# Performance work log

Measured on AMD Instinct MI355X. Metric: run time of the kernel, lower is better.

## Reference

```python
import jax, jax.numpy as jnp
import numpy as np

B, N, D = 32, 512, 256   # sets, nodes-per-set, feature dim
NUM = 4                  # badmm iterations
EPS = 1e-8


def setup_inputs() -> dict:
    key = jax.random.key(0)
    ks = jax.random.split(key, 6)
    x = jax.random.normal(ks[0], (B * N, D), dtype=jnp.float32)
    # equal-size sets: to_dense_batch(x, batch) == reshape(B, N, D), mask = all ones
    batch = jnp.repeat(jnp.arange(B, dtype=jnp.int32), N)
    # learned (num,)-shaped parameters (rho/a0..a3 = None branch: 0.1*randn(num))
    a0_p = 0.1 * jax.random.normal(ks[1], (NUM,), dtype=jnp.float32)
    a1_p = 0.1 * jax.random.normal(ks[2], (NUM,), dtype=jnp.float32)
    a2_p = 0.1 * jax.random.normal(ks[3], (NUM,), dtype=jnp.float32)
    a3_p = 0.1 * jax.random.normal(ks[4], (NUM,), dtype=jnp.float32)
    rho_p = 0.1 * jax.random.normal(ks[5], (NUM,), dtype=jnp.float32)
    return {"x": x, "a0_p": a0_p, "a1_p": a1_p, "a2_p": a2_p,
            "a3_p": a3_p, "rho_p": rho_p, "batch": batch}


def _badmm_e(xd, c1, c2, p0, q0, a0, a1, a2, a3, rho, mask):
    """Log-domain Bregman ADMM for the regularized OT pooling problem
    (f_method='badmm-e').  T (B,N,D) is the transport between N samples and
    D feature slots; S is the ADMM auxiliary copy; mu/eta are the relaxed
    row/column marginals with KL priors q0/p0; z,z1,z2 are scaled duals."""
    log_p0 = jnp.log(p0 + EPS)            # (B,1,D)
    log_q0 = jnp.log(q0 + EPS)            # (B,N,1)
    log_t = log_q0 + log_p0               # (B,N,D)
    log_s = log_t
    log_mu = log_q0                       # (B,N,1) row marginal
    log_eta = log_p0                      # (B,1,D) column marginal
    z = jnp.zeros_like(log_t)
    z1 = jnp.zeros_like(log_q0)
    z2 = jnp.zeros_like(log_p0)
    neg = jnp.where(mask > 0, 0.0, -1e9)  # (B,N,1) bias masking padded rows
    for k in range(NUM):
        # T-update: rows of T sum to mu -> softmax over feature dim (axis=2)
        gw = a1[k] * jnp.einsum('bnm,bmd,bde->bne', c2, jnp.exp(log_s), c1)
        y = (xd + gw + z + rho[k] * log_s) / (rho[k] + a0[k])
        log_t = log_mu + jax.nn.log_softmax(y, axis=2)
        # S-update: columns of S sum to eta -> softmax over sample dim (axis=1)
        gw2 = a1[k] * jnp.einsum('bnm,bmd,bde->bne', c2, jnp.exp(log_t), c1)
        y2 = (gw2 - z + rho[k] * log_t) / rho[k] + neg
        log_s = log_eta + jax.nn.log_softmax(y2, axis=1)
        # marginal prox updates (KL to priors q0/p0)
        log_t1 = jax.scipy.special.logsumexp(log_t, axis=2, keepdims=True)        # (B,N,1)
        log_mu = (a2[k] * log_q0 + rho[k] * log_t1 - z1) / (a2[k] + rho[k])
        log_s1 = jax.scipy.special.logsumexp(log_s + neg, axis=1, keepdims=True)  # (B,1,D)
        log_eta = (a3[k] * log_p0 + rho[k] * log_s1 - z2) / (a3[k] + rho[k])
        # dual ascent
        z = z + rho[k] * (jnp.exp(log_t) - jnp.exp(log_s))
        z1 = z1 + rho[k] * (jnp.exp(log_mu) - jnp.exp(log_t1))
        z2 = z2 + rho[k] * (jnp.exp(log_eta) - jnp.exp(log_s1))
    return jnp.exp(log_t)


def reference(x, a0_p, a1_p, a2_p, a3_p, rho_p, batch):
    # batch = repeat(arange(B), N): equal-size sets, to_dense_batch == reshape
    xd = x.reshape(B, N, D)
    mask = jnp.ones((B, N, 1), dtype=x.dtype)
    q0 = mask / N                              # fixed q0: segment-softmax of zeros
    p0 = jnp.ones((B, 1, D), dtype=x.dtype) / D
    c1 = jnp.einsum('bnd,bne->bde', xd, xd) / N   # (B,D,D), x^T x / N
    c2 = jnp.einsum('bnd,bmd->bnm', xd, xd) / D   # (B,N,N), x x^T / D
    c1 = c1 / jnp.max(c1)
    c2 = c2 / jnp.max(c2)
    sp = jax.nn.softplus
    trans = _badmm_e(xd, c1, c2, p0, q0, sp(a0_p), sp(a1_p), sp(a2_p),
                     sp(a3_p), sp(rho_p), mask)
    frot = D * xd * trans * mask               # (B,N,D)
    return jnp.sum(frot, axis=1)               # (B,D)
```

## Files before the change

kernel.cpp:

```cpp
#include <hip/hip_runtime.h>
#include <math.h>

#define BATCH 32
#define NN 512
#define DD 256
#define NUMK 4

typedef __attribute__((ext_vector_type(8))) short bf16x8;
typedef __attribute__((ext_vector_type(4))) float f32x4;
typedef __attribute__((ext_vector_type(4))) unsigned short u16x4;

__device__ __forceinline__ float softplusf(float v) { return log1pf(expf(v)); }

__device__ __forceinline__ unsigned enc_key(float v) {
  unsigned u = __float_as_uint(v);
  return (u & 0x80000000u) ? ~u : (u | 0x80000000u);
}
__device__ __forceinline__ float dec_key(unsigned k) {
  return (k & 0x80000000u) ? __uint_as_float(k & 0x7fffffffu) : __uint_as_float(~k);
}
__device__ __forceinline__ unsigned short f2b(float f) {
  unsigned u = __float_as_uint(f);
  unsigned r = (u + 0x7fffu + ((u >> 16) & 1u)) >> 16;
  return (unsigned short)r;
}
__device__ __forceinline__ float b2f(unsigned short h) {
  return __uint_as_float(((unsigned)h) << 16);
}

#define GLDS(gp, lp)                                                   \
  __builtin_amdgcn_global_load_lds(                                    \
      (__attribute__((address_space(1))) void*)(void*)(gp),            \
      (__attribute__((address_space(3))) void*)(lp), 16, 0, 0)

__global__ __launch_bounds__(256) void k_prep(const float* __restrict__ x,
                                              short* __restrict__ xb,
                                              short* __restrict__ xTb,
                                              unsigned* keys) {
  __shared__ float t[64][65];
  int b = blockIdx.z, n0 = blockIdx.y * 64, d0 = blockIdx.x * 64;
  if (blockIdx.x == 0 && blockIdx.y == 0 && blockIdx.z == 0 && threadIdx.x == 0) {
    keys[0] = 0u; keys[1] = 0u;
  }
  const float* X = x + (size_t)b * NN * DD;
  int col = threadIdx.x & 63, rr = threadIdx.x >> 6;
#pragma unroll
  for (int s = 0; s < 16; ++s) {
    int row = s * 4 + rr;
    float v = X[(size_t)(n0 + row) * DD + d0 + col];
    t[row][col] = v;
    xb[(size_t)b * NN * DD + (size_t)(n0 + row) * DD + d0 + col] = (short)f2b(v);
  }
  __syncthreads();
#pragma unroll
  for (int s = 0; s < 16; ++s) {
    int row = s * 4 + rr;
    xTb[(size_t)b * DD * NN + (size_t)(d0 + row) * NN + n0 + col] = (short)f2b(t[col][row]);
  }
}

template <int K, int OUTK>
__global__ __launch_bounds__(256) void k_gemm(
    const short* __restrict__ A, size_t sA, int lda,
    const short* __restrict__ Bp, size_t sB, int ldb,
    void* __restrict__ outp, size_t sO, int ldo,
    float scale, unsigned* maxslot, const float* __restrict__ P, int kiter) {
  __shared__ short As[64 * 64];
  __shared__ short Bs[64 * 64];
  const int b = blockIdx.x;
  const int m0 = blockIdx.y * 64, n0 = blockIdx.z * 64;
  const int tid = threadIdx.x, wave = tid >> 6, lane = tid & 63;
  const int ln = lane & 15, kg = lane >> 4;
  const int wr = (wave >> 1) * 32, wc = (wave & 1) * 32;
  const short* Ab = A + (size_t)b * sA;
  const short* Bb = Bp + (size_t)b * sB;

  f32x4 acc[2][2];
#pragma unroll
  for (int i = 0; i < 2; ++i)
#pragma unroll
    for (int j = 0; j < 2; ++j) acc[i][j] = (f32x4){0.f, 0.f, 0.f, 0.f};

  for (int k0 = 0; k0 < K; k0 += 64) {
    __syncthreads();
#pragma unroll
    for (int p = 0; p < 2; ++p) {
      int row = p * 32 + wave * 8 + (lane >> 3);
      int sg = (lane & 7) ^ (row & 7);
      GLDS(Ab + (size_t)(m0 + row) * lda + k0 + sg * 8, &As[(p * 32 + wave * 8) * 64]);
      GLDS(Bb + (size_t)(n0 + row) * ldb + k0 + sg * 8, &Bs[(p * 32 + wave * 8) * 64]);
    }
    __syncthreads();
    bf16x8 af[2][2], bfr[2][2];
#pragma unroll
    for (int i = 0; i < 2; ++i)
#pragma unroll
      for (int kk = 0; kk < 2; ++kk) {
        int rowA = wr + i * 16 + ln;
        af[i][kk] = *(const bf16x8*)&As[rowA * 64 + (((kk * 4 + kg) ^ (rowA & 7)) * 8)];
        int rowB = wc + i * 16 + ln;
        bfr[i][kk] = *(const bf16x8*)&Bs[rowB * 64 + (((kk * 4 + kg) ^ (rowB & 7)) * 8)];
      }
#pragma unroll
    for (int kk = 0; kk < 2; ++kk)
#pragma unroll
      for (int i = 0; i < 2; ++i)
#pragma unroll
        for (int j = 0; j < 2; ++j)
          acc[i][j] = __builtin_amdgcn_mfma_f32_16x16x32_bf16(af[i][kk], bfr[j][kk],
                                                              acc[i][j], 0, 0, 0);
  }

  unsigned short* ot = (unsigned short*)outp + (size_t)b * sO;
  if (OUTK != 1) {
    float sc = (OUTK >= 2) ? P[4 + kiter] * (1.0f / DD) : scale;
    float tmax = -1e30f;
#pragma unroll
    for (int i = 0; i < 2; ++i) {
      int r0 = m0 + wr + i * 16 + kg * 4;
#pragma unroll
      for (int j = 0; j < 2; ++j) {
        int c = n0 + wc + j * 16 + ln;
        u16x4 pk;
#pragma unroll
        for (int q = 0; q < 4; ++q) {
          float v = acc[i][j][q] * sc;
          if (OUTK == 3 && c == r0 + q) v += 1.0f;
          if (OUTK == 0) tmax = fmaxf(tmax, v);
          pk[q] = f2b(v);
        }
        *(u16x4*)&ot[(size_t)c * ldo + r0] = pk;
      }
    }
    if (OUTK == 0) {
#pragma unroll
      for (int o = 32; o > 0; o >>= 1) tmax = fmaxf(tmax, __shfl_xor(tmax, o));
      __syncthreads();
      float* smf = (float*)As;
      if (lane == 0) smf[wave] = tmax;
      __syncthreads();
      if (tid == 0)
        atomicMax(maxslot, enc_key(fmaxf(fmaxf(smf[0], smf[1]), fmaxf(smf[2], smf[3]))));
    }
  } else {
#pragma unroll
    for (int i = 0; i < 2; ++i)
#pragma unroll
      for (int j = 0; j < 2; ++j) {
        int c = n0 + wc + j * 16 + ln;
#pragma unroll
        for (int q = 0; q < 4; ++q) {
          int r = m0 + wr + i * 16 + kg * 4 + q;
          ot[(size_t)r * ldo + c] = f2b(acc[i][j][q]);
        }
      }
  }
}

__global__ __launch_bounds__(256) void k_c2max(const short* __restrict__ xb,
                                               unsigned* maxslot) {
  if (blockIdx.y > blockIdx.z) return;
  __shared__ short As[64 * 64];
  __shared__ short Bs[64 * 64];
  const int b = blockIdx.x;
  const int m0 = blockIdx.y * 64, n0 = blockIdx.z * 64;
  const int tid = threadIdx.x, wave = tid >> 6, lane = tid & 63;
  const int ln = lane & 15, kg = lane >> 4;
  const int wr = (wave >> 1) * 32, wc = (wave & 1) * 32;
  const short* Ab = xb + (size_t)b * ((size_t)NN * DD);

  f32x4 acc[2][2];
#pragma unroll
  for (int i = 0; i < 2; ++i)
#pragma unroll
    for (int j = 0; j < 2; ++j) acc[i][j] = (f32x4){0.f, 0.f, 0.f, 0.f};

  for (int k0 = 0; k0 < DD; k0 += 64) {
    __syncthreads();
#pragma unroll
    for (int p = 0; p < 2; ++p) {
      int row = p * 32 + wave * 8 + (lane >> 3);
      int sg = (lane & 7) ^ (row & 7);
      GLDS(Ab + (size_t)(m0 + row) * DD + k0 + sg * 8, &As[(p * 32 + wave * 8) * 64]);
      GLDS(Ab + (size_t)(n0 + row) * DD + k0 + sg * 8, &Bs[(p * 32 + wave * 8) * 64]);
    }
    __syncthreads();
    bf16x8 af[2][2], bfr[2][2];
#pragma unroll
    for (int i = 0; i < 2; ++i)
#pragma unroll
      for (int kk = 0; kk < 2; ++kk) {
        int rowA = wr + i * 16 + ln;
        af[i][kk] = *(const bf16x8*)&As[rowA * 64 + (((kk * 4 + kg) ^ (rowA & 7)) * 8)];
        int rowB = wc + i * 16 + ln;
        bfr[i][kk] = *(const bf16x8*)&Bs[rowB * 64 + (((kk * 4 + kg) ^ (rowB & 7)) * 8)];
      }
#pragma unroll
    for (int kk = 0; kk < 2; ++kk)
#pragma unroll
      for (int i = 0; i < 2; ++i)
#pragma unroll
        for (int j = 0; j < 2; ++j)
          acc[i][j] = __builtin_amdgcn_mfma_f32_16x16x32_bf16(af[i][kk], bfr[j][kk],
                                                              acc[i][j], 0, 0, 0);
  }
  float tmax = -1e30f;
#pragma unroll
  for (int i = 0; i < 2; ++i)
#pragma unroll
    for (int j = 0; j < 2; ++j)
#pragma unroll
      for (int q = 0; q < 4; ++q) tmax = fmaxf(tmax, acc[i][j][q] * (1.0f / DD));
#pragma unroll
  for (int o = 32; o > 0; o >>= 1) tmax = fmaxf(tmax, __shfl_xor(tmax, o));
  __syncthreads();
  float* smf = (float*)As;
  if (lane == 0) smf[wave] = tmax;
  __syncthreads();
  if (tid == 0)
    atomicMax(maxslot, enc_key(fmaxf(fmaxf(smf[0], smf[1]), fmaxf(smf[2], smf[3]))));
}

__global__ __launch_bounds__(256) void k_misc(const short* __restrict__ c1b,
                                              const short* __restrict__ xb,
                                              float* __restrict__ s1,
                                              float* __restrict__ S,
                                              const float* a0p, const float* a1p,
                                              const float* a2p, const float* a3p,
                                              const float* rhop, float* P,
                                              const unsigned* keys) {
  int bid = blockIdx.x;
  int lane = threadIdx.x & 63;
  if (bid < 2048) {
    int row = bid * 4 + (threadIdx.x >> 6);
    u16x4 v = *(const u16x4*)(c1b + (size_t)row * 256 + lane * 4);
    float s = 0.f;
#pragma unroll
    for (int q = 0; q < 4; ++q) s += b2f(v[q]);
#pragma unroll
    for (int o = 32; o > 0; o >>= 1) s += __shfl_xor(s, o);
    if (lane == 0) s1[row] = s;
  } else if (bid < 2080) {
    int b = bid - 2048;
    int d = threadIdx.x;
    const short* X = xb + (size_t)b * NN * DD;
    float s = 0.f;
    for (int n = 0; n < NN; ++n) s += b2f((unsigned short)X[(size_t)n * DD + d]);
    S[(size_t)b * DD + d] = s;
  } else if (threadIdx.x == 0) {
    float M1 = dec_key(keys[0]);
    float M2 = dec_key(keys[1]);
    float lq0 = logf(1.0f / NN + 1e-8f);
    float lp0 = logf(1.0f / DD + 1e-8f);
    float mu = lq0, eta = lp0, z1 = 0.f, z2 = 0.f;
    for (int k = 0; k < NUMK; ++k) {
      float a0 = softplusf(a0p[k]), a1 = softplusf(a1p[k]);
      float a2 = softplusf(a2p[k]), a3 = softplusf(a3p[k]);
      float rho = softplusf(rhop[k]);
      P[0 + k] = a0;
      P[4 + k] = a1 / (M1 * M2);
      P[8 + k] = rho;
      P[12 + k] = mu;
      P[16 + k] = eta;
      float t1 = mu;
      mu = (a2 * lq0 + rho * t1 - z1) / (a2 + rho);
      z1 += rho * (expf(mu) - expf(t1));
      float s1v = eta;
      eta = (a3 * lp0 + rho * s1v - z2) / (a3 + rho);
      z2 += rho * (expf(eta) - expf(s1v));
    }
  }
}

__global__ __launch_bounds__(512) void k_tsm0(
    const short* __restrict__ xTb, const float* __restrict__ S,
    const float* __restrict__ s1, short* __restrict__ eTT,
    const float* __restrict__ P) {
  const int b = blockIdx.x, n0 = blockIdx.y * 64;
  const int nl = threadIdx.x >> 3, ds = threadIdx.x & 7;
  const int n = n0 + nl;
  const size_t base = (size_t)b * ((size_t)NN * DD);
  float y[32];
  float dot = 0.f;
#pragma unroll
  for (int dk = 0; dk < 32; ++dk) {
    int d = dk * 8 + ds;
    float v = b2f((unsigned short)xTb[base + (size_t)d * NN + n]);
    y[dk] = v;
    dot += v * S[(size_t)b * DD + d];
  }
  dot += __shfl_xor(dot, 1);
  dot += __shfl_xor(dot, 2);
  dot += __shfl_xor(dot, 4);
  const float c0 = logf(1.0f / NN + 1e-8f) + logf(1.0f / DD + 1e-8f);
  float g = P[4] * expf(c0) * dot * (1.0f / DD);
  float inv = 1.0f / (P[8] + P[0]);
  float m = -1e30f;
#pragma unroll
  for (int dk = 0; dk < 32; ++dk) {
    int d = dk * 8 + ds;
    y[dk] = (y[dk] + g * s1[(size_t)b * DD + d]) * inv;
    m = fmaxf(m, y[dk]);
  }
  m = fmaxf(m, __shfl_xor(m, 1));
  m = fmaxf(m, __shfl_xor(m, 2));
  m = fmaxf(m, __shfl_xor(m, 4));
  float s = 0.f;
#pragma unroll
  for (int dk = 0; dk < 32; ++dk) s += expf(y[dk] - m);
  s += __shfl_xor(s, 1);
  s += __shfl_xor(s, 2);
  s += __shfl_xor(s, 4);
  const float lse = m + logf(s);
  const float mu = P[12];
#pragma unroll
  for (int dk = 0; dk < 32; ++dk) {
    int d = dk * 8 + ds;
    eTT[base + (size_t)d * NN + n] = (short)f2b(expf(mu + y[dk] - lse));
  }
}

template <int LAST>
__global__ __launch_bounds__(256) void k_ft(
    const short* __restrict__ xb, const short* __restrict__ Mtb,
    const short* __restrict__ eST, const short* __restrict__ zb,
    short* __restrict__ eTT, const short* __restrict__ xTb,
    float* __restrict__ part, const float* __restrict__ P, int kiter) {
  __shared__ short As[32 * 64];
  __shared__ short Bs[256 * 64];
  const int b = blockIdx.x, m0 = blockIdx.y * 32;
  const int tid = threadIdx.x, wave = tid >> 6, lane = tid & 63;
  const int ln = lane & 15, kg = lane >> 4;
  const short* Ab = xb + (size_t)b * ((size_t)NN * DD);
  const short* Bb = Mtb + (size_t)b * ((size_t)DD * DD);
  const size_t base = (size_t)b * ((size_t)NN * DD);

  f32x4 acc[2][4];
#pragma unroll
  for (int i = 0; i < 2; ++i)
#pragma unroll
    for (int j = 0; j < 4; ++j) acc[i][j] = (f32x4){0.f, 0.f, 0.f, 0.f};

  for (int k0 = 0; k0 < DD; k0 += 64) {
    __syncthreads();
    {
      int row = wave * 8 + (lane >> 3);
      int sg = (lane & 7) ^ (row & 7);
      GLDS(Ab + (size_t)(m0 + row) * DD + k0 + sg * 8, &As[(wave * 8) * 64]);
    }
#pragma unroll
    for (int c = 0; c < 8; ++c) {
      int row = wave * 64 + c * 8 + (lane >> 3);
      int sg = (lane & 7) ^ (row & 7);
      GLDS(Bb + (size_t)row * DD + k0 + sg * 8, &Bs[(wave * 64 + c * 8) * 64]);
    }
    __syncthreads();
    bf16x8 af[2][2], bfr[4][2];
#pragma unroll
    for (int i = 0; i < 2; ++i)
#pragma unroll
      for (int kk = 0; kk < 2; ++kk) {
        int rowA = i * 16 + ln;
        af[i][kk] = *(const bf16x8*)&As[rowA * 64 + (((kk * 4 + kg) ^ (rowA & 7)) * 8)];
      }
#pragma unroll
    for (int j = 0; j < 4; ++j)
#pragma unroll
      for (int kk = 0; kk < 2; ++kk) {
        int rowB = wave * 64 + j * 16 + ln;
        bfr[j][kk] = *(const bf16x8*)&Bs[rowB * 64 + (((kk * 4 + kg) ^ (rowB & 7)) * 8)];
      }
#pragma unroll
    for (int kk = 0; kk < 2; ++kk)
#pragma unroll
      for (int i = 0; i < 2; ++i)
#pragma unroll
        for (int j = 0; j < 4; ++j)
          acc[i][j] = __builtin_amdgcn_mfma_f32_16x16x32_bf16(af[i][kk], bfr[j][kk],
                                                              acc[i][j], 0, 0, 0);
  }
  __syncthreads();
  float* red = (float*)As;

  const float a0 = P[kiter], rho = P[8 + kiter], mu = P[12 + kiter];
  const float inv = 1.0f / (rho + a0);
  float y[2][4][4];
#pragma unroll
  for (int i = 0; i < 2; ++i)
#pragma unroll
    for (int j = 0; j < 4; ++j) {
      int d = wave * 64 + j * 16 + ln;
      int n4 = m0 + i * 16 + kg * 4;
      size_t idx = base + (size_t)d * NN + n4;
      u16x4 zv = *(const u16x4*)&zb[idx];
      u16x4 es = *(const u16x4*)&eST[idx];
#pragma unroll
      for (int q = 0; q < 4; ++q)
        y[i][j][q] = (acc[i][j][q] + b2f(zv[q]) + rho * logf(b2f(es[q]))) * inv;
    }
  float pm[2][4];
#pragma unroll
  for (int i = 0; i < 2; ++i)
#pragma unroll
    for (int q = 0; q < 4; ++q) {
      float m = fmaxf(fmaxf(y[i][0][q], y[i][1][q]), fmaxf(y[i][2][q], y[i][3][q]));
      m = fmaxf(m, __shfl_xor(m, 1));
      m = fmaxf(m, __shfl_xor(m, 2));
      m = fmaxf(m, __shfl_xor(m, 4));
      m = fmaxf(m, __shfl_xor(m, 8));
      pm[i][q] = m;
    }
  if (ln == 0) {
#pragma unroll
    for (int i = 0; i < 2; ++i)
#pragma unroll
      for (int q = 0; q < 4; ++q) red[wave * 32 + i * 16 + kg * 4 + q] = pm[i][q];
  }
  __syncthreads();
  if (tid < 32)
    red[128 + tid] = fmaxf(fmaxf(red[tid], red[32 + tid]),
                           fmaxf(red[64 + tid], red[96 + tid]));
  __syncthreads();
  float sm[2][4], mc[2][4];
#pragma unroll
  for (int i = 0; i < 2; ++i)
#pragma unroll
    for (int q = 0; q < 4; ++q) {
      mc[i][q] = red[128 + i * 16 + kg * 4 + q];
      float s = expf(y[i][0][q] - mc[i][q]) + expf(y[i][1][q] - mc[i][q]) +
                expf(y[i][2][q] - mc[i][q]) + expf(y[i][3][q] - mc[i][q]);
      s += __shfl_xor(s, 1);
      s += __shfl_xor(s, 2);
      s += __shfl_xor(s, 4);
      s += __shfl_xor(s, 8);
      sm[i][q] = s;
    }
  __syncthreads();
  if (ln == 0) {
#pragma unroll
    for (int i = 0; i < 2; ++i)
#pragma unroll
      for (int q = 0; q < 4; ++q) red[wave * 32 + i * 16 + kg * 4 + q] = sm[i][q];
  }
  __syncthreads();
  if (tid < 32)
    red[160 + tid] = red[128 + tid] +
                     logf(red[tid] + red[32 + tid] + red[64 + tid] + red[96 + tid]);
  __syncthreads();
  float lse[2][4];
#pragma unroll
  for (int i = 0; i < 2; ++i)
#pragma unroll
    for (int q = 0; q < 4; ++q) lse[i][q] = red[160 + i * 16 + kg * 4 + q];

  if (LAST == 0) {
#pragma unroll
    for (int i = 0; i < 2; ++i)
#pragma unroll
      for (int j = 0; j < 4; ++j) {
        int d = wave * 64 + j * 16 + ln;
        int n4 = m0 + i * 16 + kg * 4;
        size_t idx = base + (size_t)d * NN + n4;
        u16x4 et;
#pragma unroll
        for (int q = 0; q < 4; ++q) et[q] = f2b(expf(mu + y[i][j][q] - lse[i][q]));
        *(u16x4*)&eTT[idx] = et;
      }
  } else {
    float p[4] = {0.f, 0.f, 0.f, 0.f};
#pragma unroll
    for (int j = 0; j < 4; ++j)
#pragma unroll
      for (int i = 0; i < 2; ++i) {
        int d = wave * 64 + j * 16 + ln;
        int n4 = m0 + i * 16 + kg * 4;
        size_t idx = base + (size_t)d * NN + n4;
        u16x4 xv = *(const u16x4*)&xTb[idx];
#pragma unroll
        for (int q = 0; q < 4; ++q)
          p[j] += b2f(xv[q]) * expf(mu + y[i][j][q] - lse[i][q]);
      }
#pragma unroll
    for (int j = 0; j < 4; ++j) {
      p[j] += __shfl_xor(p[j], 16);
      p[j] += __shfl_xor(p[j], 32);
    }
    if (kg == 0) {
      size_t pb = ((size_t)b * 16 + blockIdx.y) * DD;
#pragma unroll
      for (int j = 0; j < 4; ++j) part[pb + wave * 64 + j * 16 + ln] = p[j];
    }
  }
}

template <int ZFIRST>
__global__ __launch_bounds__(512) void k_fs(
    const short* __restrict__ xb, const short* __restrict__ Mtb,
    const short* __restrict__ eTT, short* __restrict__ eST,
    short* __restrict__ zb, const float* __restrict__ P, int kiter) {
  __shared__ short As[512 * 32];
  __shared__ short Bs[32 * 32];
  const int b = blockIdx.x, m0 = blockIdx.y * 32;
  const int tid = threadIdx.x, wave = tid >> 6, lane = tid & 63;
  const int ln = lane & 15, kg = lane >> 4;
  const short* Ab = xb + (size_t)b * ((size_t)NN * DD);
  const short* Bb = Mtb + (size_t)b * ((size_t)DD * DD);
  const size_t base = (size_t)b * ((size_t)NN * DD);

  f32x4 acc[4][2];
#pragma unroll
  for (int i = 0; i < 4; ++i)
#pragma unroll
    for (int j = 0; j < 2; ++j) acc[i][j] = (f32x4){0.f, 0.f, 0.f, 0.f};

  for (int k0 = 0; k0 < DD; k0 += 32) {
    __syncthreads();
#pragma unroll
    for (int c = 0; c < 4; ++c) {
      int row = wave * 64 + c * 16 + (lane >> 2);
      int sg = (lane & 3) ^ (row & 3);
      GLDS(Ab + (size_t)row * DD + k0 + sg * 8, &As[(wave * 64 + c * 16) * 32]);
    }
    if (wave < 2) {
      int row = wave * 16 + (lane >> 2);
      int sg = (lane & 3) ^ (row & 3);
      GLDS(Bb + (size_t)(m0 + row) * DD + k0 + sg * 8, &Bs[(wave * 16) * 32]);
    }
    __syncthreads();
    bf16x8 af[4], bfr[2];
#pragma unroll
    for (int i = 0; i < 4; ++i) {
      int rowA = wave * 64 + i * 16 + ln;
      af[i] = *(const bf16x8*)&As[rowA * 32 + ((kg ^ (rowA & 3)) * 8)];
    }
#pragma unroll
    for (int j = 0; j < 2; ++j) {
      int rowB = j * 16 + ln;
      bfr[j] = *(const bf16x8*)&Bs[rowB * 32 + ((kg ^ (rowB & 3)) * 8)];
    }
#pragma unroll
    for (int i = 0; i < 4; ++i)
#pragma unroll
      for (int j = 0; j < 2; ++j)
        acc[i][j] = __builtin_amdgcn_mfma_f32_16x16x32_bf16(af[i], bfr[j], acc[i][j], 0, 0, 0);
  }
  __syncthreads();
  float* red = (float*)Bs;

  const float rho = P[8 + kiter], eta = P[16 + kiter];
  const float invr = 1.0f / rho;
  float y[4][2][4];
  u16x4 etr[4][2], zr[4][2];
#pragma unroll
  for (int i = 0; i < 4; ++i)
#pragma unroll
    for (int j = 0; j < 2; ++j) {
      int d = m0 + j * 16 + ln;
      int n4 = wave * 64 + i * 16 + kg * 4;
      size_t idx = base + (size_t)d * NN + n4;
      etr[i][j] = *(const u16x4*)&eTT[idx];
      if (!ZFIRST) zr[i][j] = *(const u16x4*)&zb[idx];
#pragma unroll
      for (int q = 0; q < 4; ++q) {
        float zf = ZFIRST ? 0.0f : b2f(zr[i][j][q]);
        y[i][j][q] = (acc[i][j][q] - zf + rho * logf(b2f(etr[i][j][q]))) * invr;
      }
    }
  float pm[2];
#pragma unroll
  for (int j = 0; j < 2; ++j) {
    float m = -1e30f;
#pragma unroll
    for (int i = 0; i < 4; ++i)
#pragma unroll
      for (int q = 0; q < 4; ++q) m = fmaxf(m, y[i][j][q]);
    m = fmaxf(m, __shfl_xor(m, 16));
    m = fmaxf(m, __shfl_xor(m, 32));
    pm[j] = m;
  }
  if (kg == 0) {
#pragma unroll
    for (int j = 0; j < 2; ++j) red[wave * 32 + j * 16 + ln] = pm[j];
  }
  __syncthreads();
  if (tid < 32) {
    float M = red[tid];
#pragma unroll
    for (int w = 1; w < 8; ++w) M = fmaxf(M, red[w * 32 + tid]);
    red[256 + tid] = M;
  }
  __syncthreads();
  float mc[2], ps[2];
#pragma unroll
  for (int j = 0; j < 2; ++j) {
    mc[j] = red[256 + j * 16 + ln];
    float s = 0.f;
#pragma unroll
    for (int i = 0; i < 4; ++i)
#pragma unroll
      for (int q = 0; q < 4; ++q) s += expf(y[i][j][q] - mc[j]);
    s += __shfl_xor(s, 16);
    s += __shfl_xor(s, 32);
    ps[j] = s;
  }
  __syncthreads();
  if (kg == 0) {
#pragma unroll
    for (int j = 0; j < 2; ++j) red[wave * 32 + j * 16 + ln] = ps[j];
  }
  __syncthreads();
  if (tid < 32) {
    float S = 0.f;
#pragma unroll
    for (int w = 0; w < 8; ++w) S += red[w * 32 + tid];
    red[288 + tid] = red[256 + tid] + logf(S);
  }
  __syncthreads();
  float lse[2];
#pragma unroll
  for (int j = 0; j < 2; ++j) lse[j] = red[288 + j * 16 + ln];

#pragma unroll
  for (int i = 0; i < 4; ++i)
#pragma unroll
    for (int j = 0; j < 2; ++j) {
      int d = m0 + j * 16 + ln;
      int n4 = wave * 64 + i * 16 + kg * 4;
      size_t idx = base + (size_t)d * NN + n4;
      u16x4 ev, zo;
#pragma unroll
      for (int q = 0; q < 4; ++q) {
        float es = expf(eta + y[i][j][q] - lse[j]);
        ev[q] = f2b(es);
        float zf = ZFIRST ? 0.0f : b2f(zr[i][j][q]);
        zo[q] = f2b(zf + rho * (b2f(etr[i][j][q]) - es));
      }
      *(u16x4*)&eST[idx] = ev;
      *(u16x4*)&zb[idx] = zo;
    }
}

__global__ __launch_bounds__(256) void k_out2(const float* __restrict__ part,
                                              float* __restrict__ out) {
  int b = blockIdx.x, d = threadIdx.x;
  float acc = 0.0f;
#pragma unroll
  for (int c = 0; c < 16; ++c) acc += part[((size_t)b * 16 + c) * DD + d];
  out[(size_t)b * DD + d] = (float)DD * acc;
}

extern "C" void kernel_launch(void* const* d_in, const int* in_sizes, int n_in,
                              void* d_out, int out_size, void* d_ws, size_t ws_size,
                              hipStream_t stream) {
  const float* x = (const float*)d_in[0];
  const float* a0p = (const float*)d_in[1];
  const float* a1p = (const float*)d_in[2];
  const float* a2p = (const float*)d_in[3];
  const float* a3p = (const float*)d_in[4];
  const float* rhop = (const float*)d_in[5];
  float* out = (float*)d_out;

  const size_t NE = (size_t)BATCH * NN * DD;
  const size_t NE_b = (size_t)NN * DD;
  const size_t C1_b = (size_t)DD * DD;

  float* fws = (float*)d_ws;
  float* S = fws;
  float* s1 = S + BATCH * DD;
  float* part = s1 + BATCH * DD;
  float* P = part + BATCH * 16 * DD;
  unsigned* keys = (unsigned*)(P + 24);
  short* sws = (short*)(keys + 8);
  short* xb = sws;
  short* xTb = sws + NE;
  short* eTT = sws + 2 * NE;
  short* eST = sws + 3 * NE;
  short* zb = sws + 4 * NE;
  short* Fb = sws + 5 * NE;
  short* Mtb = Fb + (size_t)BATCH * C1_b;
  short* c1b = Mtb + (size_t)BATCH * C1_b;

  k_prep<<<dim3(4, 8, BATCH), 256, 0, stream>>>(x, xb, xTb, keys);
  k_gemm<512, 0><<<dim3(BATCH, 4, 4), 256, 0, stream>>>(
      xTb, NE_b, NN, xTb, NE_b, NN, (void*)c1b, C1_b, DD, 1.0f / NN, keys + 0,
      nullptr, 0);
  k_c2max<<<dim3(BATCH, 8, 8), 256, 0, stream>>>(xb, keys + 1);
  k_misc<<<2081, 256, 0, stream>>>(c1b, xb, s1, S, a0p, a1p, a2p, a3p, rhop, P, keys);

  k_tsm0<<<dim3(BATCH, 8), 512, 0, stream>>>(xTb, S, s1, eTT, P);
  k_gemm<512, 1><<<dim3(BATCH, 4, 4), 256, 0, stream>>>(
      xTb, NE_b, NN, eTT, NE_b, NN, (void*)Fb, C1_b, DD, 1.0f, nullptr, nullptr, 0);
  k_gemm<256, 2><<<dim3(BATCH, 4, 4), 256, 0, stream>>>(
      Fb, C1_b, DD, c1b, C1_b, DD, (void*)Mtb, C1_b, DD, 0.f, nullptr, P, 0);
  k_fs<1><<<dim3(BATCH, 8), 512, 0, stream>>>(xb, Mtb, eTT, eST, zb, P, 0);

  for (int k = 1; k <= 2; ++k) {
    k_gemm<512, 1><<<dim3(BATCH, 4, 4), 256, 0, stream>>>(
        xTb, NE_b, NN, eST, NE_b, NN, (void*)Fb, C1_b, DD, 1.0f, nullptr, nullptr, 0);
    k_gemm<256, 3><<<dim3(BATCH, 4, 4), 256, 0, stream>>>(
        Fb, C1_b, DD, c1b, C1_b, DD, (void*)Mtb, C1_b, DD, 0.f, nullptr, P, k);
    k_ft<0><<<dim3(BATCH, 16), 256, 0, stream>>>(xb, Mtb, eST, zb, eTT, xTb,
                                                 part, P, k);
    k_gemm<512, 1><<<dim3(BATCH, 4, 4), 256, 0, stream>>>(
        xTb, NE_b, NN, eTT, NE_b, NN, (void*)Fb, C1_b, DD, 1.0f, nullptr, nullptr, 0);
    k_gemm<256, 2><<<dim3(BATCH, 4, 4), 256, 0, stream>>>(
        Fb, C1_b, DD, c1b, C1_b, DD, (void*)Mtb, C1_b, DD, 0.f, nullptr, P, k);
    k_fs<0><<<dim3(BATCH, 8), 512, 0, stream>>>(xb, Mtb, eTT, eST, zb, P, k);
  }

  k_gemm<512, 1><<<dim3(BATCH, 4, 4), 256, 0, stream>>>(
      xTb, NE_b, NN, eST, NE_b, NN, (void*)Fb, C1_b, DD, 1.0f, nullptr, nullptr, 0);
  k_gemm<256, 3><<<dim3(BATCH, 4, 4), 256, 0, stream>>>(
      Fb, C1_b, DD, c1b, C1_b, DD, (void*)Mtb, C1_b, DD, 0.f, nullptr, P, 3);
  k_ft<1><<<dim3(BATCH, 16), 256, 0, stream>>>(xb, Mtb, eST, zb, eTT, xTb,
                                               part, P, 3);
  k_out2<<<BATCH, 256, 0, stream>>>(part, out);
}
```

Baseline: 246.5 us.

## Fuse chained F and M GEMMs into one kernel and merge Gram kernels

Replaces each pair of GEMM launches (F = x^T·E, then M = F·c1 scaled) with a single kernel where each block computes a 64-row stripe of F into LDS and immediately multiplies it by c1. This removes the F round-trip through global memory and one launch per pair. The c1 and c2-max Gram kernels are also merged into a single launch with a job index. In exchange, the fused kernel launches only 128 blocks (down from 512 per GEMM) and uses more LDS per block, which may leave compute units idle.

Result: slower. 341.0 us (+38.3%).

```diff
diff --git a/kernel.cpp b/kernel.cpp
--- a/kernel.cpp
+++ b/kernel.cpp
@@ -59,21 +59,40 @@
   }
 }
 
-template <int K, int OUTK>
-__global__ __launch_bounds__(256) void k_gemm(
-    const short* __restrict__ A, size_t sA, int lda,
-    const short* __restrict__ Bp, size_t sB, int ldb,
-    void* __restrict__ outp, size_t sO, int ldo,
-    float scale, unsigned* maxslot, const float* __restrict__ P, int kiter) {
+__global__ __launch_bounds__(256) void k_gram(const short* __restrict__ xb,
+                                              const short* __restrict__ xTb,
+                                              short* __restrict__ c1b,
+                                              unsigned* keys) {
   __shared__ short As[64 * 64];
   __shared__ short Bs[64 * 64];
   const int b = blockIdx.x;
-  const int m0 = blockIdx.y * 64, n0 = blockIdx.z * 64;
+  const int job = blockIdx.y;
   const int tid = threadIdx.x, wave = tid >> 6, lane = tid & 63;
   const int ln = lane & 15, kg = lane >> 4;
   const int wr = (wave >> 1) * 32, wc = (wave & 1) * 32;
-  const short* Ab = A + (size_t)b * sA;
-  const short* Bb = Bp + (size_t)b * sB;
+  const bool isC1 = job < 16;
+  int m0, n0, K, lda;
+  const short* Ab;
+  if (isC1) {
+    m0 = (job >> 2) * 64;
+    n0 = (job & 3) * 64;
+    K = NN;
+    lda = NN;
+    Ab = xTb + (size_t)b * ((size_t)NN * DD);
+  } else {
+    int jj = job - 16;
+    int r = 0, accu = 0;
+    for (; r < 8; ++r) {
+      int cnt = 8 - r;
+      if (jj < accu + cnt) break;
+      accu += cnt;
+    }
+    m0 = r * 64;
+    n0 = (r + jj - accu) * 64;
+    K = DD;
+    lda = DD;
+    Ab = xb + (size_t)b * ((size_t)NN * DD);
+  }
 
   f32x4 acc[2][2];
 #pragma unroll
@@ -88,7 +107,7 @@
       int row = p * 32 + wave * 8 + (lane >> 3);
       int sg = (lane & 7) ^ (row & 7);
       GLDS(Ab + (size_t)(m0 + row) * lda + k0 + sg * 8, &As[(p * 32 + wave * 8) * 64]);
-      GLDS(Bb + (size_t)(n0 + row) * ldb + k0 + sg * 8, &Bs[(p * 32 + wave * 8) * 64]);
+      GLDS(Ab + (size_t)(n0 + row) * lda + k0 + sg * 8, &Bs[(p * 32 + wave * 8) * 64]);
     }
     __syncthreads();
     bf16x8 af[2][2], bfr[2][2];
@@ -111,10 +130,10 @@
                                                               acc[i][j], 0, 0, 0);
   }
 
-  unsigned short* ot = (unsigned short*)outp + (size_t)b * sO;
-  if (OUTK != 1) {
-    float sc = (OUTK >= 2) ? P[4 + kiter] * (1.0f / DD) : scale;
-    float tmax = -1e30f;
+  const float sc = isC1 ? (1.0f / NN) : (1.0f / DD);
+  float tmax = -1e30f;
+  if (isC1) {
+    unsigned short* ot = (unsigned short*)c1b + (size_t)b * ((size_t)DD * DD);
 #pragma unroll
     for (int i = 0; i < 2; ++i) {
       int r0 = m0 + wr + i * 16 + kg * 4;
@@ -125,92 +144,20 @@
 #pragma unroll
         for (int q = 0; q < 4; ++q) {
           float v = acc[i][j][q] * sc;
-          if (OUTK == 3 && c == r0 + q) v += 1.0f;
-          if (OUTK == 0) tmax = fmaxf(tmax, v);
+          tmax = fmaxf(tmax, v);
           pk[q] = f2b(v);
         }
-        *(u16x4*)&ot[(size_t)c * ldo + r0] = pk;
-      }
-    }
-    if (OUTK == 0) {
-#pragma unroll
-      for (int o = 32; o > 0; o >>= 1) tmax = fmaxf(tmax, __shfl_xor(tmax, o));
-      __syncthreads();
-      float* smf = (float*)As;
-      if (lane == 0) smf[wave] = tmax;
-      __syncthreads();
-      if (tid == 0)
-        atomicMax(maxslot, enc_key(fmaxf(fmaxf(smf[0], smf[1]), fmaxf(smf[2], smf[3]))));
+        *(u16x4*)&ot[(size_t)c * DD + r0] = pk;
+      }
     }
   } else {
 #pragma unroll
     for (int i = 0; i < 2; ++i)
 #pragma unroll
-      for (int j = 0; j < 2; ++j) {
-        int c = n0 + wc + j * 16 + ln;
-#pragma unroll
-        for (int q = 0; q < 4; ++q) {
-          int r = m0 + wr + i * 16 + kg * 4 + q;
-          ot[(size_t)r * ldo + c] = f2b(acc[i][j][q]);
-        }
-      }
-  }
-}
-
-__global__ __launch_bounds__(256) void k_c2max(const short* __restrict__ xb,
-                                               unsigned* maxslot) {
-  if (blockIdx.y > blockIdx.z) return;
-  __shared__ short As[64 * 64];
-  __shared__ short Bs[64 * 64];
-  const int b = blockIdx.x;
-  const int m0 = blockIdx.y * 64, n0 = blockIdx.z * 64;
-  const int tid = threadIdx.x, wave = tid >> 6, lane = tid & 63;
-  const int ln = lane & 15, kg = lane >> 4;
-  const int wr = (wave >> 1) * 32, wc = (wave & 1) * 32;
-  const short* Ab = xb + (size_t)b * ((size_t)NN * DD);
-
-  f32x4 acc[2][2];
-#pragma unroll
-  for (int i = 0; i < 2; ++i)
-#pragma unroll
-    for (int j = 0; j < 2; ++j) acc[i][j] = (f32x4){0.f, 0.f, 0.f, 0.f};
-
-  for (int k0 = 0; k0 < DD; k0 += 64) {
-    __syncthreads();
-#pragma unroll
-    for (int p = 0; p < 2; ++p) {
-      int row = p * 32 + wave * 8 + (lane >> 3);
-      int sg = (lane & 7) ^ (row & 7);
-      GLDS(Ab + (size_t)(m0 + row) * DD + k0 + sg * 8, &As[(p * 32 + wave * 8) * 64]);
-      GLDS(Ab + (size_t)(n0 + row) * DD + k0 + sg * 8, &Bs[(p * 32 + wave * 8) * 64]);
-    }
-    __syncthreads();
-    bf16x8 af[2][2], bfr[2][2];
-#pragma unroll
-    for (int i = 0; i < 2; ++i)
-#pragma unroll
-      for (int kk = 0; kk < 2; ++kk) {
-        int rowA = wr + i * 16 + ln;
-        af[i][kk] = *(const bf16x8*)&As[rowA * 64 + (((kk * 4 + kg) ^ (rowA & 7)) * 8)];
-        int rowB = wc + i * 16 + ln;
-        bfr[i][kk] = *(const bf16x8*)&Bs[rowB * 64 + (((kk * 4 + kg) ^ (rowB & 7)) * 8)];
-      }
-#pragma unroll
-    for (int kk = 0; kk < 2; ++kk)
-#pragma unroll
-      for (int i = 0; i < 2; ++i)
-#pragma unroll
-        for (int j = 0; j < 2; ++j)
-          acc[i][j] = __builtin_amdgcn_mfma_f32_16x16x32_bf16(af[i][kk], bfr[j][kk],
-                                                              acc[i][j], 0, 0, 0);
-  }
-  float tmax = -1e30f;
-#pragma unroll
-  for (int i = 0; i < 2; ++i)
-#pragma unroll
-    for (int j = 0; j < 2; ++j)
-#pragma unroll
-      for (int q = 0; q < 4; ++q) tmax = fmaxf(tmax, acc[i][j][q] * (1.0f / DD));
+      for (int j = 0; j < 2; ++j)
+#pragma unroll
+        for (int q = 0; q < 4; ++q) tmax = fmaxf(tmax, acc[i][j][q] * sc);
+  }
 #pragma unroll
   for (int o = 32; o > 0; o >>= 1) tmax = fmaxf(tmax, __shfl_xor(tmax, o));
   __syncthreads();
@@ -218,7 +165,8 @@
   if (lane == 0) smf[wave] = tmax;
   __syncthreads();
   if (tid == 0)
-    atomicMax(maxslot, enc_key(fmaxf(fmaxf(smf[0], smf[1]), fmaxf(smf[2], smf[3]))));
+    atomicMax(keys + (isC1 ? 0 : 1),
+              enc_key(fmaxf(fmaxf(smf[0], smf[1]), fmaxf(smf[2], smf[3]))));
 }
 
 __global__ __launch_bounds__(256) void k_misc(const short* __restrict__ c1b,
@@ -320,6 +268,127 @@
   }
 }
 
+template <int OUTM>
+__global__ __launch_bounds__(256) void k_fm(
+    const short* __restrict__ xTb, const short* __restrict__ E,
+    const short* __restrict__ c1b, short* __restrict__ Mtb,
+    const float* __restrict__ P, int kiter) {
+  __shared__ short As[64 * 64];
+  __shared__ short Bs[64 * 64];
+  __shared__ short Fl[64 * 256];
+  const int b = blockIdx.x, m0 = blockIdx.y * 64;
+  const int tid = threadIdx.x, wave = tid >> 6, lane = tid & 63;
+  const int ln = lane & 15, kg = lane >> 4;
+  const int wr = (wave >> 1) * 32, wc = (wave & 1) * 32;
+  const short* Ab = xTb + (size_t)b * ((size_t)NN * DD);
+  const short* Eb = E + (size_t)b * ((size_t)NN * DD);
+  const short* Cb = c1b + (size_t)b * ((size_t)DD * DD);
+
+  for (int cc = 0; cc < 4; ++cc) {
+    f32x4 acc[2][2];
+#pragma unroll
+    for (int i = 0; i < 2; ++i)
+#pragma unroll
+      for (int j = 0; j < 2; ++j) acc[i][j] = (f32x4){0.f, 0.f, 0.f, 0.f};
+    for (int k0 = 0; k0 < NN; k0 += 64) {
+      __syncthreads();
+#pragma unroll
+      for (int p = 0; p < 2; ++p) {
+        int row = p * 32 + wave * 8 + (lane >> 3);
+        int sg = (lane & 7) ^ (row & 7);
+        GLDS(Ab + (size_t)(m0 + row) * NN + k0 + sg * 8, &As[(p * 32 + wave * 8) * 64]);
+        GLDS(Eb + (size_t)(cc * 64 + row) * NN + k0 + sg * 8, &Bs[(p * 32 + wave * 8) * 64]);
+      }
+      __syncthreads();
+      bf16x8 af[2][2], bfr[2][2];
+#pragma unroll
+      for (int i = 0; i < 2; ++i)
+#pragma unroll
+        for (int kk = 0; kk < 2; ++kk) {
+          int rowA = wr + i * 16 + ln;
+          af[i][kk] = *(const bf16x8*)&As[rowA * 64 + (((kk * 4 + kg) ^ (rowA & 7)) * 8)];
+          int rowB = wc + i * 16 + ln;
+          bfr[i][kk] = *(const bf16x8*)&Bs[rowB * 64 + (((kk * 4 + kg) ^ (rowB & 7)) * 8)];
+        }
+#pragma unroll
+      for (int kk = 0; kk < 2; ++kk)
+#pragma unroll
+        for (int i = 0; i < 2; ++i)
+#pragma unroll
+          for (int j = 0; j < 2; ++j)
+            acc[i][j] = __builtin_amdgcn_mfma_f32_16x16x32_bf16(af[i][kk], bfr[j][kk],
+                                                                acc[i][j], 0, 0, 0);
+    }
+#pragma unroll
+    for (int i = 0; i < 2; ++i)
+#pragma unroll
+      for (int j = 0; j < 2; ++j) {
+        int c = cc * 64 + wc + j * 16 + ln;
+#pragma unroll
+        for (int q = 0; q < 4; ++q) {
+          int r = wr + i * 16 + kg * 4 + q;
+          Fl[r * 256 + ((((c >> 3) ^ (r & 7)) << 3) + (c & 7))] = (short)f2b(acc[i][j][q]);
+        }
+      }
+  }
+  __syncthreads();
+
+  const float sc = P[4 + kiter] * (1.0f / DD);
+  unsigned short* ot = (unsigned short*)Mtb + (size_t)b * ((size_t)DD * DD);
+  for (int cc = 0; cc < 4; ++cc) {
+    f32x4 acc[2][2];
+#pragma unroll
+    for (int i = 0; i < 2; ++i)
+#pragma unroll
+      for (int j = 0; j < 2; ++j) acc[i][j] = (f32x4){0.f, 0.f, 0.f, 0.f};
+    for (int k0 = 0; k0 < DD; k0 += 64) {
+      __syncthreads();
+#pragma unroll
+      for (int p = 0; p < 2; ++p) {
+        int row = p * 32 + wave * 8 + (lane >> 3);
+        int sg = (lane & 7) ^ (row & 7);
+        GLDS(Cb + (size_t)(cc * 64 + row) * DD + k0 + sg * 8, &Bs[(p * 32 + wave * 8) * 64]);
+      }
+      __syncthreads();
+      bf16x8 af[2][2], bfr[2][2];
+#pragma unroll
+      for (int i = 0; i < 2; ++i)
+#pragma unroll
+        for (int kk = 0; kk < 2; ++kk) {
+          int rowA = wr + i * 16 + ln;
+          int kchunk = (k0 >> 3) + kk * 4 + kg;
+          af[i][kk] = *(const bf16x8*)&Fl[rowA * 256 + ((kchunk ^ (rowA & 7)) << 3)];
+          int rowB = wc + i * 16 + ln;
+          bfr[i][kk] = *(const bf16x8*)&Bs[rowB * 64 + (((kk * 4 + kg) ^ (rowB & 7)) * 8)];
+        }
+#pragma unroll
+      for (int kk = 0; kk < 2; ++kk)
+#pragma unroll
+        for (int i = 0; i < 2; ++i)
+#pragma unroll
+          for (int j = 0; j < 2; ++j)
+            acc[i][j] = __builtin_amdgcn_mfma_f32_16x16x32_bf16(af[i][kk], bfr[j][kk],
+                                                                acc[i][j], 0, 0, 0);
+    }
+#pragma unroll
+    for (int i = 0; i < 2; ++i) {
+      int r0 = m0 + wr + i * 16 + kg * 4;
+#pragma unroll
+      for (int j = 0; j < 2; ++j) {
+        int c = cc * 64 + wc + j * 16 + ln;
+        u16x4 pk;
+#pragma unroll
+        for (int q = 0; q < 4; ++q) {
+          float v = acc[i][j][q] * sc;
+          if (OUTM == 1 && c == r0 + q) v += 1.0f;
+          pk[q] = f2b(v);
+        }
+        *(u16x4*)&ot[(size_t)c * DD + r0] = pk;
+      }
+    }
+  }
+}
+
 template <int LAST>
 __global__ __launch_bounds__(256) void k_ft(
     const short* __restrict__ xb, const short* __restrict__ Mtb,
@@ -661,7 +730,6 @@
   float* out = (float*)d_out;
 
   const size_t NE = (size_t)BATCH * NN * DD;
-  const size_t NE_b = (size_t)NN * DD;
   const size_t C1_b = (size_t)DD * DD;
 
   float* fws = (float*)d_ws;
@@ -676,42 +744,26 @@
   short* eTT = sws + 2 * NE;
   short* eST = sws + 3 * NE;
   short* zb = sws + 4 * NE;
-  short* Fb = sws + 5 * NE;
-  short* Mtb = Fb + (size_t)BATCH * C1_b;
+  short* Mtb = sws + 5 * NE;
   short* c1b = Mtb + (size_t)BATCH * C1_b;
 
   k_prep<<<dim3(4, 8, BATCH), 256, 0, stream>>>(x, xb, xTb, keys);
-  k_gemm<512, 0><<<dim3(BATCH, 4, 4), 256, 0, stream>>>(
-      xTb, NE_b, NN, xTb, NE_b, NN, (void*)c1b, C1_b, DD, 1.0f / NN, keys + 0,
-      nullptr, 0);
-  k_c2max<<<dim3(BATCH, 8, 8), 256, 0, stream>>>(xb, keys + 1);
+  k_gram<<<dim3(BATCH, 52), 256, 0, stream>>>(xb, xTb, c1b, keys);
   k_misc<<<2081, 256, 0, stream>>>(c1b, xb, s1, S, a0p, a1p, a2p, a3p, rhop, P, keys);
 
   k_tsm0<<<dim3(BATCH, 8), 512, 0, stream>>>(xTb, S, s1, eTT, P);
-  k_gemm<512, 1><<<dim3(BATCH, 4, 4), 256, 0, stream>>>(
-      xTb, NE_b, NN, eTT, NE_b, NN, (void*)Fb, C1_b, DD, 1.0f, nullptr, nullptr, 0);
-  k_gemm<256, 2><<<dim3(BATCH, 4, 4), 256, 0, stream>>>(
-      Fb, C1_b, DD, c1b, C1_b, DD, (void*)Mtb, C1_b, DD, 0.f, nullptr, P, 0);
+  k_fm<0><<<dim3(BATCH, 4), 256, 0, stream>>>(xTb, eTT, c1b, Mtb, P, 0);
   k_fs<1><<<dim3(BATCH, 8), 512, 0, stream>>>(xb, Mtb, eTT, eST, zb, P, 0);
 
   for (int k = 1; k <= 2; ++k) {
-    k_gemm<512, 1><<<dim3(BATCH, 4, 4), 256, 0, stream>>>(
-        xTb, NE_b, NN, eST, NE_b, NN, (void*)Fb, C1_b, DD, 1.0f, nullptr, nullptr, 0);
-    k_gemm<256, 3><<<dim3(BATCH, 4, 4), 256, 0, stream>>>(
-        Fb, C1_b, DD, c1b, C1_b, DD, (void*)Mtb, C1_b, DD, 0.f, nullptr, P, k);
+    k_fm<1><<<dim3(BATCH, 4), 256, 0, stream>>>(xTb, eST, c1b, Mtb, P, k);
     k_ft<0><<<dim3(BATCH, 16), 256, 0, stream>>>(xb, Mtb, eST, zb, eTT, xTb,
                                                  part, P, k);
-    k_gemm<512, 1><<<dim3(BATCH, 4, 4), 256, 0, stream>>>(
-        xTb, NE_b, NN, eTT, NE_b, NN, (void*)Fb, C1_b, DD, 1.0f, nullptr, nullptr, 0);
-    k_gemm<256, 2><<<dim3(BATCH, 4, 4), 256, 0, stream>>>(
-        Fb, C1_b, DD, c1b, C1_b, DD, (void*)Mtb, C1_b, DD, 0.f, nullptr, P, k);
+    k_fm<0><<<dim3(BATCH, 4), 256, 0, stream>>>(xTb, eTT, c1b, Mtb, P, k);
     k_fs<0><<<dim3(BATCH, 8), 512, 0, stream>>>(xb, Mtb, eTT, eST, zb, P, k);
   }
 
-  k_gemm<512, 1><<<dim3(BATCH, 4, 4), 256, 0, stream>>>(
-      xTb, NE_b, NN, eST, NE_b, NN, (void*)Fb, C1_b, DD, 1.0f, nullptr, nullptr, 0);
-  k_gemm<256, 3><<<dim3(BATCH, 4, 4), 256, 0, stream>>>(
-      Fb, C1_b, DD, c1b, C1_b, DD, (void*)Mtb, C1_b, DD, 0.f, nullptr, P, 3);
+  k_fm<1><<<dim3(BATCH, 4), 256, 0, stream>>>(xTb, eST, c1b, Mtb, P, 3);
   k_ft<1><<<dim3(BATCH, 16), 256, 0, stream>>>(xb, Mtb, eST, zb, eTT, xTb,
                                                part, P, 3);
   k_out2<<<BATCH, 256, 0, stream>>>(part, out);
```
